# Optimization experiments

Measured on AMD Instinct MI355X. Metric: run time of the kernel, lower is better.

Reference implementation:

```python
import jax, jax.numpy as jnp
import numpy as np
from jax import lax

B, A, H, W = 64, 8, 64, 128
T_EXP = 32
ACTION_HORIZON = 64
DS = 1.0          # reward_cfg['ds']
TEMPERATURE = 0.1 # policy_kwargs['temperature'], method='sharpen'
FOV_HALF_ANGLE_DEG = 35.0
FOV_MAX_RANGE = 100


def _build_buffers():
    # per-action 3x3 one-hot transition kernels: weight 1.0 at 'center' cell,
    # 0.0 at left/right cells (as in MaxEntIRL.__init__ with policy_method='pp')
    center = [[2, 2], [2, 1], [2, 0], [1, 2], [1, 0], [0, 2], [0, 1], [0, 0]]
    tp = np.zeros((A, 1, 3, 3), np.float32)
    for i, (r, c) in enumerate(center):
        tp[i, 0, r, c] = 1.0
    # trapezoidal FOV mask built on a (2H, W) grid, then cropped to first H rows
    rows = np.arange(2 * H, dtype=np.float32)[:, None]
    cols = np.arange(W, dtype=np.float32)[None, :]
    half = np.tan(np.deg2rad(FOV_HALF_ANGLE_DEG)) * rows
    mask = ((np.abs(cols - (W - 1) / 2.0) <= half) & (rows <= FOV_MAX_RANGE))
    fov = mask.astype(np.float32)[:H][None, None]  # (1,1,H,W)
    dyn = np.array([[-1, -1], [-1, 0], [-1, 1], [0, -1],
                    [0, 1], [1, -1], [1, 0], [1, 1]], np.int32)
    return jnp.asarray(tp), jnp.asarray(fov), jnp.asarray(dyn)


def setup_inputs() -> dict:
    key = jax.random.key(0)
    k1, k2 = jax.random.split(key)
    policy = jax.random.normal(k1, (B, A, H, W), jnp.float32)
    # expert SE(2)-like poses; only [:, :, :2, 2] translations are read.
    # Scale to [0,100) so grid cells spread over the map before clamping.
    expert = jax.random.uniform(k2, (B, T_EXP, 3, 3), jnp.float32) * 100.0
    tp, fov, dyn = _build_buffers()
    return {"policy": policy, "expert": expert, "transition_probs": tp,
            "fov_mask": fov, "dynamics": dyn, "action_horizon": ACTION_HORIZON}


def reference(policy, expert, transition_probs, fov_mask, dynamics, action_horizon):
    Bn, An, Hn, Wn = policy.shape
    n_states = Hn * Wn
    barange = jnp.arange(Bn)

    # expert poses -> clamped grid cells  (S: (B, T, 2))
    S = jnp.floor_divide(expert[:, :, :2, 2], DS).astype(jnp.int32)
    S = jnp.stack([jnp.clip(S[..., 0], 0, Hn - 1),
                   jnp.clip(S[..., 1], 0, Wn - 1)], axis=-1)

    # earliest pose inside FOV (argmax of bool gives first True, else 0)
    mask2d = fov_mask[0, 0]
    in_fov = mask2d[S[..., 0], S[..., 1]] > 0  # (B, T)
    idx0 = jnp.argmax(in_fov, axis=1)
    S0c = S[barange, idx0]     # (B, 2) start cell
    S1c = S[:, -1]             # (B, 2) terminal cell
    S0 = S0c[:, 0] * Wn + S0c[:, 1]
    S1 = S1c[:, 0] * Wn + S1c[:, 1]

    # sharpen policy over action dim (stable softmax with temperature)
    logits = (policy - jnp.max(policy, axis=1, keepdims=True)) / TEMPERATURE
    policy_2d = jax.nn.softmax(logits, axis=1)  # (B, A, H, W)

    mu0 = jnp.zeros((Bn, n_states), jnp.float32).at[barange, S0].set(1.0)

    def step(carry, _):
        prev, total = carry
        # zero_terminal_state: kill visitation mass at the terminal cell
        prev_z = prev.at[barange, S1].set(0.0)
        pm = policy_2d * prev_z.reshape(Bn, 1, Hn, Wn)  # (B, A, H, W)
        new = lax.conv_general_dilated(
            pm, transition_probs, window_strides=(1, 1),
            padding=[(1, 1), (1, 1)],
            dimension_numbers=("NCHW", "OIHW", "NCHW"),
            feature_group_count=An)
        new = jnp.sum(new, axis=1).reshape(Bn, n_states)
        return (new, total + prev_z), None

    (last, total), _ = lax.scan(step, (mu0, jnp.zeros_like(mu0)),
                                None, length=action_horizon - 1)
    mu = (total + last).reshape(Bn, Hn, Wn)

    # greedy rollout (torch runs this under no_grad)
    policy_flat = policy.reshape(Bn, An, n_states)
    most_likely_action = jnp.argmax(policy_flat, axis=1)  # (B, n_states)
    most_likely_action = lax.stop_gradient(most_likely_action)

    def roll(St, _):
        a = most_likely_action[barange, St]
        coord = jnp.stack([St // Wn, St % Wn], axis=1) + dynamics[a]
        coord = jnp.stack([jnp.clip(coord[:, 0], 0, Hn - 1),
                           jnp.clip(coord[:, 1], 0, Wn - 1)], axis=1)
        return coord[:, 0] * Wn + coord[:, 1], coord

    _, coords = lax.scan(roll, S0, None, length=action_horizon - 1)  # (T-1,B,2)
    states = jnp.concatenate([S0c[None].astype(coords.dtype), coords],
                             axis=0).transpose(1, 0, 2)  # (B, T, 2)
    bidx = jnp.broadcast_to(barange[:, None], (Bn, action_horizon))
    states_grid = jnp.zeros((Bn, Hn, Wn), jnp.float32).at[
        bidx, states[..., 0], states[..., 1]].add(1.0)
    return mu, states_grid, states
```

## Files before the change

kernel.cpp:

```cpp
#include <hip/hip_runtime.h>

#define THREADS 512

typedef unsigned int u32;

constexpr int BN = 64, AN = 8, HN = 64, WN = 128;
constexpr int HWN = HN * WN;
constexpr int TEXP = 32, AH = 64;
constexpr int PSTR = 136, PROWS = 66;
constexpr int PGUARD = 8;
constexpr int PBUF = PGUARD + PROWS * PSTR;
constexpr size_t LDS_BYTES = (size_t)AN * HWN * 2;

constexpr int GYc[8] = { 1, 1, 1, 0, 0, -1, -1, -1 };
constexpr int GXc[8] = { 1, 0, -1, 1, -1, 1, 0, -1 };

typedef _Float16 h2 __attribute__((ext_vector_type(2)));

union V4 { uint4 q; u32 u[4]; h2 p[4]; _Float16 h[8]; };

__device__ __forceinline__ u32 ab16(u32 hi, u32 lo) {
    return (u32)((((unsigned long long)hi << 32) | lo) >> 16);
}

__device__ __forceinline__ void shiftLR(const V4& d, u32 eLhi, u32 eRlo, V4& L, V4& R) {
    u32 m1 = ab16(d.u[1], d.u[0]);
    u32 m2 = ab16(d.u[2], d.u[1]);
    u32 m3 = ab16(d.u[3], d.u[2]);
    L.u[0] = ab16(d.u[0], eLhi); L.u[1] = m1; L.u[2] = m2; L.u[3] = m3;
    R.u[0] = m1; R.u[1] = m2; R.u[2] = m3; R.u[3] = ab16(eRlo, d.u[3]);
}

extern "C" __global__ __launch_bounds__(THREADS, 2)
void maxent_fused(const float* __restrict__ policy,
                  const float* __restrict__ expert,
                  const float* __restrict__ fovm,
                  const int*   __restrict__ dyn,
                  float* __restrict__ out)
{
    (void)dyn;
    extern __shared__ char smem[];
    const int tid  = threadIdx.x;
    const int lane = tid & 63;
    const bool isScan = blockIdx.x < BN;
    const int b = isScan ? (int)blockIdx.x : (int)blockIdx.x - BN;

    int Sr = 0, Sc = 0; bool infov = false;
    if (lane < TEXP) {
        float e0 = expert[b * (TEXP * 9) + lane * 9 + 2];
        float e1 = expert[b * (TEXP * 9) + lane * 9 + 5];
        int r = (int)floorf(e0); r = r < 0 ? 0 : (r > HN - 1 ? HN - 1 : r);
        int c = (int)floorf(e1); c = c < 0 ? 0 : (c > WN - 1 ? WN - 1 : c);
        Sr = r; Sc = c;
        infov = fovm[r * WN + c] > 0.0f;
    }
    unsigned long long fmask = __ballot(infov);
    int idx0 = fmask ? (__ffsll(fmask) - 1) : 0;
    const int S0r = __shfl(Sr, idx0), S0c = __shfl(Sc, idx0);
    const int S1r = __shfl(Sr, TEXP - 1), S1c = __shfl(Sc, TEXP - 1);
    const bool S0eqS1 = (S0r == S1r) && (S0c == S1c);

    if (isScan) {
        _Float16* Pl = (_Float16*)smem;

        const float* pb = policy + (size_t)b * AN * HWN;
        #pragma unroll
        for (int kk = 0; kk < 4; ++kk) {
            const int pix = (kk * THREADS + tid) * 4;
            float v[8][4];
            float m[4] = {-3.4e38f, -3.4e38f, -3.4e38f, -3.4e38f};
            #pragma unroll
            for (int a = 0; a < 8; ++a) {
                float4 f = *(const float4*)(pb + a * HWN + pix);
                v[a][0] = f.x; v[a][1] = f.y; v[a][2] = f.z; v[a][3] = f.w;
                m[0] = fmaxf(m[0], f.x); m[1] = fmaxf(m[1], f.y);
                m[2] = fmaxf(m[2], f.z); m[3] = fmaxf(m[3], f.w);
            }
            float s[4] = {0.f, 0.f, 0.f, 0.f};
            #pragma unroll
            for (int a = 0; a < 8; ++a)
                #pragma unroll
                for (int j = 0; j < 4; ++j) { v[a][j] = __expf((v[a][j] - m[j]) * 10.0f); s[j] += v[a][j]; }
            float inv[4];
            #pragma unroll
            for (int j = 0; j < 4; ++j) inv[j] = 1.0f / s[j];
            #pragma unroll
            for (int a = 0; a < 8; ++a) {
                u32 lo = (u32)__builtin_bit_cast(unsigned short, (_Float16)(v[a][0] * inv[0]))
                       | ((u32)__builtin_bit_cast(unsigned short, (_Float16)(v[a][1] * inv[1])) << 16);
                u32 hi = (u32)__builtin_bit_cast(unsigned short, (_Float16)(v[a][2] * inv[2]))
                       | ((u32)__builtin_bit_cast(unsigned short, (_Float16)(v[a][3] * inv[3])) << 16);
                uint2 pk2; pk2.x = lo; pk2.y = hi;
                *(uint2*)(Pl + a * HWN + pix) = pk2;
            }
        }
        __syncthreads();

        const int wv = tid >> 6;
        const int y0 = 8 * wv + 2 * (lane >> 4);
        const int x0 = (lane & 15) * 8;
        const bool edgeL = (lane & 15) == 0;
        const bool edgeR = (lane & 15) == 15;

        V4 pa0[8], pa1[8];
        #pragma unroll
        for (int a = 0; a < 8; ++a) {
            const int gy = GYc[a], gx = GXc[a];
            #pragma unroll
            for (int r = 0; r < 2; ++r) {
                const int ny = y0 + r + gy;
                V4 wvv;
                #pragma unroll
                for (int k = 0; k < 8; ++k) wvv.h[k] = (_Float16)0.0f;
                if (ny >= 0 && ny < HN) {
                    const _Float16* base = Pl + a * HWN + ny * WN + x0;
                    V4 qq; qq.q = *(const uint4*)base;
                    if (gx == 0) {
                        wvv = qq;
                    } else if (gx == 1) {
                        _Float16 e = (x0 < WN - 8) ? base[8] : base[7];
                        #pragma unroll
                        for (int k = 0; k < 7; ++k) wvv.h[k] = qq.h[k + 1];
                        wvv.h[7] = e;
                    } else {
                        _Float16 e = (x0 > 0) ? base[-1] : base[0];
                        wvv.h[0] = e;
                        #pragma unroll
                        for (int k = 1; k < 8; ++k) wvv.h[k] = qq.h[k - 1];
                    }
                }
                if (r == 0) pa0[a] = wvv; else pa1[a] = wvv;
            }
        }
        __syncthreads();

        _Float16* B0 = (_Float16*)smem;
        _Float16* B1 = B0 + PBUF;
        for (int i = tid; i < 2 * PBUF; i += THREADS) B0[i] = (_Float16)0.0f;
        __syncthreads();
        if (tid == 0 && !S0eqS1) B0[PGUARD + (S0r + 1) * PSTR + S0c] = (_Float16)1.0f;
        __syncthreads();

        const bool own0 = (y0     == S1r) && (S1c >= x0) && (S1c < x0 + 8);
        const bool own1 = (y0 + 1 == S1r) && (S1c >= x0) && (S1c < x0 + 8);
        V4 zA, zB, sA, sB;
        #pragma unroll
        for (int q = 0; q < 4; ++q) {
            u32 mA = ~0u, mB = ~0u;
            if (own0 && ((S1c - x0) >> 1) == q) mA = ((S1c - x0) & 1) ? 0x0000FFFFu : 0xFFFF0000u;
            if (own1 && ((S1c - x0) >> 1) == q) mB = ((S1c - x0) & 1) ? 0x0000FFFFu : 0xFFFF0000u;
            zA.u[q] = mA; zB.u[q] = mB;
            u32 v0 = 0;
            if (!S0eqS1 && y0 == S0r && S0c >= x0 && S0c < x0 + 8 && ((S0c - x0) >> 1) == q)
                v0 = ((S0c - x0) & 1) ? 0x3C000000u : 0x00003C00u;
            u32 v1 = 0;
            if (!S0eqS1 && y0 + 1 == S0r && S0c >= x0 && S0c < x0 + 8 && ((S0c - x0) >> 1) == q)
                v1 = ((S0c - x0) & 1) ? 0x3C000000u : 0x00003C00u;
            sA.u[q] = v0; sB.u[q] = v1;
        }

        float total[16];
        #pragma unroll
        for (int k = 0; k < 16; ++k) total[k] = 0.f;
        V4 nnA, nnB;
        #pragma unroll
        for (int q = 0; q < 4; ++q) { nnA.u[q] = 0; nnB.u[q] = 0; }

        const int offT  = PGUARD + y0 * PSTR + x0;
        const int offD  = offT + 3 * PSTR;
        const int offW0 = offT + PSTR;
        const int offW1 = offW0 + PSTR;

        _Float16* RB = B0; _Float16* WB = B1;
        for (int it = 0; it < AH - 1; ++it) {
            const bool active = (8 * wv <= S0r + it + 1) && (8 * wv + 7 >= S0r - it - 1);
            if (active) {
                V4 qT, qD;
                qT.q = *(const uint4*)(RB + offT);
                qD.q = *(const uint4*)(RB + offD);

                #pragma unroll
                for (int q = 0; q < 4; ++q) {
                    total[2*q]     += (float)sA.p[q].x;
                    total[2*q + 1] += (float)sA.p[q].y;
                    total[8 + 2*q]     += (float)sB.p[q].x;
                    total[8 + 2*q + 1] += (float)sB.p[q].y;
                }

                u32 packL_AB = (sA.u[3] >> 16) | (sB.u[3] & 0xFFFF0000u);
                u32 packR_AB = (sA.u[0] & 0xFFFFu) | (sB.u[0] << 16);
                u32 packL_TD = (qT.u[3] >> 16) | (qD.u[3] & 0xFFFF0000u);
                u32 packR_TD = (qT.u[0] & 0xFFFFu) | (qD.u[0] << 16);
                u32 pLab = (u32)__shfl((int)packL_AB, (lane - 1) & 63); pLab = edgeL ? 0u : pLab;
                u32 pRab = (u32)__shfl((int)packR_AB, (lane + 1) & 63); pRab = edgeR ? 0u : pRab;
                u32 pLtd = (u32)__shfl((int)packL_TD, (lane - 1) & 63); pLtd = edgeL ? 0u : pLtd;
                u32 pRtd = (u32)__shfl((int)packR_TD, (lane + 1) & 63); pRtd = edgeR ? 0u : pRtd;

                V4 TL, TR, AL, AR, BL, BR, DL, DR;
                shiftLR(qT, pLtd << 16,          pRtd & 0xFFFFu, TL, TR);
                shiftLR(qD, pLtd & 0xFFFF0000u,  pRtd >> 16,     DL, DR);
                shiftLR(sA, pLab << 16,          pRab & 0xFFFFu, AL, AR);
                shiftLR(sB, pLab & 0xFFFF0000u,  pRab >> 16,     BL, BR);

                #pragma unroll
                for (int q = 0; q < 4; ++q) { nnA.u[q] = 0; nnB.u[q] = 0; }
                #define ACC(dst, pa, src) \
                    _Pragma("unroll") for (int q = 0; q < 4; ++q) dst.p[q] += pa.p[q] * src.p[q];
                ACC(nnA, pa0[0], BR) ACC(nnA, pa0[1], sB) ACC(nnA, pa0[2], BL)
                ACC(nnA, pa0[3], AR)                       ACC(nnA, pa0[4], AL)
                ACC(nnA, pa0[5], TR) ACC(nnA, pa0[6], qT) ACC(nnA, pa0[7], TL)
                ACC(nnB, pa1[0], DR) ACC(nnB, pa1[1], qD) ACC(nnB, pa1[2], DL)
                ACC(nnB, pa1[3], BR)                       ACC(nnB, pa1[4], BL)
                ACC(nnB, pa1[5], AR) ACC(nnB, pa1[6], sA) ACC(nnB, pa1[7], AL)
                #undef ACC

                #pragma unroll
                for (int q = 0; q < 4; ++q) {
                    sA.u[q] = nnA.u[q] & zA.u[q];
                    sB.u[q] = nnB.u[q] & zB.u[q];
                }
                *(uint4*)(WB + offW0) = sA.q;
                *(uint4*)(WB + offW1) = sB.q;
            }
            __syncthreads();
            _Float16* t = RB; RB = WB; WB = t;
        }

        float* ob0 = out + (size_t)b * HWN + y0 * WN + x0;
        float* ob1 = ob0 + WN;
        #pragma unroll
        for (int k = 0; k < 8; ++k) {
            ob0[k] = total[k]     + (float)nnA.h[k];
            ob1[k] = total[8 + k] + (float)nnB.h[k];
        }

    } else {
        short* amap = (short*)smem;
        float* grid = (float*)(smem + 16384);
        const float* pb = policy + (size_t)b * AN * HWN;
        #pragma unroll
        for (int c = 0; c < 4; ++c) {
            const int pix = (c * THREADS + tid) * 4;
            float4 f0 = *(const float4*)(pb + pix);
            float b0 = f0.x, b1 = f0.y, b2 = f0.z, b3 = f0.w;
            int a0 = 0, a1 = 0, a2 = 0, a3 = 0;
            #pragma unroll
            for (int a = 1; a < 8; ++a) {
                float4 f = *(const float4*)(pb + a * HWN + pix);
                if (f.x > b0) { b0 = f.x; a0 = a; }
                if (f.y > b1) { b1 = f.y; a1 = a; }
                if (f.z > b2) { b2 = f.z; a2 = a; }
                if (f.w > b3) { b3 = f.w; a3 = a; }
            }
            uint2 pk2;
            pk2.x = (u32)a0 | ((u32)a1 << 16);
            pk2.y = (u32)a2 | ((u32)a3 << 16);
            *(uint2*)(amap + pix) = pk2;
        }
        for (int i = tid; i < HWN; i += THREADS) grid[i] = 0.f;
        __syncthreads();

        if (tid == 0) {
            float* so = out + 2 * (size_t)HWN * BN + b * (AH * 2);
            int cr = S0r, cc = S0c;
            so[0] = (float)cr; so[1] = (float)cc;
            grid[cr * WN + cc] += 1.0f;
            for (int t = 1; t < AH; ++t) {
                const int a = amap[cr * WN + cc];
                const int dr = (a < 3) ? -1 : ((a < 5) ? 0 : 1);
                int dc;
                if (a < 3) dc = a - 1;
                else if (a == 3) dc = -1;
                else if (a == 4) dc = 1;
                else dc = a - 6;
                cr += dr; cc += dc;
                cr = cr < 0 ? 0 : (cr > HN - 1 ? HN - 1 : cr);
                cc = cc < 0 ? 0 : (cc > WN - 1 ? WN - 1 : cc);
                so[t * 2] = (float)cr; so[t * 2 + 1] = (float)cc;
                grid[cr * WN + cc] += 1.0f;
            }
        }
        __syncthreads();
        float* sg = out + (size_t)HWN * BN + b * HWN;
        for (int i = tid; i < HWN; i += THREADS) sg[i] = grid[i];
    }
}

extern "C" void kernel_launch(void* const* d_in, const int* in_sizes, int n_in,
                              void* d_out, int out_size, void* d_ws, size_t ws_size,
                              hipStream_t stream) {
    const float* policy = (const float*)d_in[0];
    const float* expert = (const float*)d_in[1];
    const float* fovm   = (const float*)d_in[3];
    const int*   dyn    = (const int*)d_in[4];
    float* out = (float*)d_out;

    (void)hipFuncSetAttribute((const void*)maxent_fused,
                              hipFuncAttributeMaxDynamicSharedMemorySize,
                              (int)LDS_BYTES);
    hipLaunchKernelGGL(maxent_fused, dim3(2 * BN), dim3(THREADS), LDS_BYTES, stream,
                       policy, expert, fovm, dyn, out);
}
```

Baseline: 56.40 us.

## Use DPP row shifts and precompute own-band stencil terms before the barrier

The cross-lane neighbour exchanges in the recurrence loop switch from __shfl to DPP row_shr/row_shl with bound_ctrl zeroing, which also handles the 16-lane row edges. The stencil contributions that depend only on the thread's own two rows are computed right after the store, before the barrier, so only the terms that need the neighbour rows (loaded from LDS) stay on the path after the barrier. Per-step totals are now summed in fp16 and flushed to fp32 every four steps, which removes conversions but adds fp16 rounding error to the accumulated totals.

```diff
diff --git a/kernel.cpp b/kernel.cpp
--- a/kernel.cpp
+++ b/kernel.cpp
@@ -29,6 +29,13 @@
     u32 m3 = ab16(d.u[3], d.u[2]);
     L.u[0] = ab16(d.u[0], eLhi); L.u[1] = m1; L.u[2] = m2; L.u[3] = m3;
     R.u[0] = m1; R.u[1] = m2; R.u[2] = m3; R.u[3] = ab16(eRlo, d.u[3]);
+}
+
+__device__ __forceinline__ u32 dpp_from_left(u32 x) {
+    return (u32)__builtin_amdgcn_update_dpp(0, (int)x, 0x111 , 0xf, 0xf, true);
+}
+__device__ __forceinline__ u32 dpp_from_right(u32 x) {
+    return (u32)__builtin_amdgcn_update_dpp(0, (int)x, 0x101 , 0xf, 0xf, true);
 }
 
 extern "C" __global__ __launch_bounds__(THREADS, 2)
@@ -99,8 +106,6 @@
         const int wv = tid >> 6;
         const int y0 = 8 * wv + 2 * (lane >> 4);
         const int x0 = (lane & 15) * 8;
-        const bool edgeL = (lane & 15) == 0;
-        const bool edgeR = (lane & 15) == 15;
 
         V4 pa0[8], pa1[8];
         #pragma unroll
@@ -162,14 +167,38 @@
         float total[16];
         #pragma unroll
         for (int k = 0; k < 16; ++k) total[k] = 0.f;
-        V4 nnA, nnB;
-        #pragma unroll
-        for (int q = 0; q < 4; ++q) { nnA.u[q] = 0; nnB.u[q] = 0; }
+        V4 nnA, nnB, tA, tB;
+        #pragma unroll
+        for (int q = 0; q < 4; ++q) { nnA.u[q] = 0; nnB.u[q] = 0; tA.u[q] = 0; tB.u[q] = 0; }
 
         const int offT  = PGUARD + y0 * PSTR + x0;
         const int offD  = offT + 3 * PSTR;
         const int offW0 = offT + PSTR;
         const int offW1 = offW0 + PSTR;
+
+        #define COMPUTE_OWN(ownA_, ownB_)                                              \
+        {                                                                              \
+            u32 packL = (sA.u[3] >> 16) | (sB.u[3] & 0xFFFF0000u);                     \
+            u32 packR = (sA.u[0] & 0xFFFFu) | (sB.u[0] << 16);                         \
+            u32 pL = dpp_from_left(packL);                                             \
+            u32 pR = dpp_from_right(packR);                                            \
+            V4 AL, AR, BL, BR;                                                         \
+            shiftLR(sA, pL << 16,          pR & 0xFFFFu, AL, AR);                      \
+            shiftLR(sB, pL & 0xFFFF0000u,  pR >> 16,     BL, BR);                      \
+            _Pragma("unroll")                                                          \
+            for (int q = 0; q < 4; ++q) {                                              \
+                h2 a = pa0[0].p[q] * BR.p[q]; a += pa0[1].p[q] * sB.p[q];              \
+                a += pa0[2].p[q] * BL.p[q];   a += pa0[3].p[q] * AR.p[q];              \
+                a += pa0[4].p[q] * AL.p[q];                                            \
+                h2 bb = pa1[3].p[q] * BR.p[q]; bb += pa1[4].p[q] * BL.p[q];            \
+                bb += pa1[5].p[q] * AR.p[q];   bb += pa1[6].p[q] * sA.p[q];            \
+                bb += pa1[7].p[q] * AL.p[q];                                           \
+                ownA_.p[q] = a; ownB_.p[q] = bb;                                       \
+            }                                                                          \
+        }
+
+        V4 ownA, ownB;
+        COMPUTE_OWN(ownA, ownB)
 
         _Float16* RB = B0; _Float16* WB = B1;
         for (int it = 0; it < AH - 1; ++it) {
@@ -180,51 +209,42 @@
                 qD.q = *(const uint4*)(RB + offD);
 
                 #pragma unroll
-                for (int q = 0; q < 4; ++q) {
-                    total[2*q]     += (float)sA.p[q].x;
-                    total[2*q + 1] += (float)sA.p[q].y;
-                    total[8 + 2*q]     += (float)sB.p[q].x;
-                    total[8 + 2*q + 1] += (float)sB.p[q].y;
+                for (int q = 0; q < 4; ++q) { tA.p[q] += sA.p[q]; tB.p[q] += sB.p[q]; }
+                if ((it & 3) == 3 || it == AH - 2) {
+                    #pragma unroll
+                    for (int q = 0; q < 4; ++q) {
+                        total[2*q]       += (float)tA.p[q].x;  total[2*q + 1]     += (float)tA.p[q].y;
+                        total[8 + 2*q]   += (float)tB.p[q].x;  total[8 + 2*q + 1] += (float)tB.p[q].y;
+                        tA.u[q] = 0; tB.u[q] = 0;
+                    }
                 }
 
-                u32 packL_AB = (sA.u[3] >> 16) | (sB.u[3] & 0xFFFF0000u);
-                u32 packR_AB = (sA.u[0] & 0xFFFFu) | (sB.u[0] << 16);
                 u32 packL_TD = (qT.u[3] >> 16) | (qD.u[3] & 0xFFFF0000u);
                 u32 packR_TD = (qT.u[0] & 0xFFFFu) | (qD.u[0] << 16);
-                u32 pLab = (u32)__shfl((int)packL_AB, (lane - 1) & 63); pLab = edgeL ? 0u : pLab;
-                u32 pRab = (u32)__shfl((int)packR_AB, (lane + 1) & 63); pRab = edgeR ? 0u : pRab;
-                u32 pLtd = (u32)__shfl((int)packL_TD, (lane - 1) & 63); pLtd = edgeL ? 0u : pLtd;
-                u32 pRtd = (u32)__shfl((int)packR_TD, (lane + 1) & 63); pRtd = edgeR ? 0u : pRtd;
-
-                V4 TL, TR, AL, AR, BL, BR, DL, DR;
+                u32 pLtd = dpp_from_left(packL_TD);
+                u32 pRtd = dpp_from_right(packR_TD);
+                V4 TL, TR, DL, DR;
                 shiftLR(qT, pLtd << 16,          pRtd & 0xFFFFu, TL, TR);
                 shiftLR(qD, pLtd & 0xFFFF0000u,  pRtd >> 16,     DL, DR);
-                shiftLR(sA, pLab << 16,          pRab & 0xFFFFu, AL, AR);
-                shiftLR(sB, pLab & 0xFFFF0000u,  pRab >> 16,     BL, BR);
-
-                #pragma unroll
-                for (int q = 0; q < 4; ++q) { nnA.u[q] = 0; nnB.u[q] = 0; }
-                #define ACC(dst, pa, src) \
-                    _Pragma("unroll") for (int q = 0; q < 4; ++q) dst.p[q] += pa.p[q] * src.p[q];
-                ACC(nnA, pa0[0], BR) ACC(nnA, pa0[1], sB) ACC(nnA, pa0[2], BL)
-                ACC(nnA, pa0[3], AR)                       ACC(nnA, pa0[4], AL)
-                ACC(nnA, pa0[5], TR) ACC(nnA, pa0[6], qT) ACC(nnA, pa0[7], TL)
-                ACC(nnB, pa1[0], DR) ACC(nnB, pa1[1], qD) ACC(nnB, pa1[2], DL)
-                ACC(nnB, pa1[3], BR)                       ACC(nnB, pa1[4], BL)
-                ACC(nnB, pa1[5], AR) ACC(nnB, pa1[6], sA) ACC(nnB, pa1[7], AL)
-                #undef ACC
-
                 #pragma unroll
                 for (int q = 0; q < 4; ++q) {
+                    h2 a = ownA.p[q] + pa0[5].p[q] * TR.p[q];
+                    a += pa0[6].p[q] * qT.p[q];  a += pa0[7].p[q] * TL.p[q];
+                    h2 bb = ownB.p[q] + pa1[0].p[q] * DR.p[q];
+                    bb += pa1[1].p[q] * qD.p[q]; bb += pa1[2].p[q] * DL.p[q];
+                    nnA.p[q] = a; nnB.p[q] = bb;
                     sA.u[q] = nnA.u[q] & zA.u[q];
                     sB.u[q] = nnB.u[q] & zB.u[q];
                 }
                 *(uint4*)(WB + offW0) = sA.q;
                 *(uint4*)(WB + offW1) = sB.q;
+
+                COMPUTE_OWN(ownA, ownB)
             }
             __syncthreads();
             _Float16* t = RB; RB = WB; WB = t;
         }
+        #undef COMPUTE_OWN
 
         float* ob0 = out + (size_t)b * HWN + y0 * WN + x0;
         float* ob1 = ob0 + WN;
```

New measurement: 52.81 us. 6.4% less time.

## Remap diffusion scan to column-pair lanes with DPP shifts and row-halo LDS exchange

Applied to the files above, without the earlier changes.

Each lane now owns two adjacent columns across eight rows instead of eight columns across two rows. Horizontal neighbours come from DPP wave shifts instead of ds shuffles, and vertical neighbours come from registers within the wave. Only the top and bottom rows of each wave go through a small double-buffered LDS halo instead of a full padded state buffer. Running totals are also accumulated in fp16 for four steps before being flushed to fp32, which saves conversions but loses some precision.

```diff
diff --git a/kernel.cpp b/kernel.cpp
--- a/kernel.cpp
+++ b/kernel.cpp
@@ -3,33 +3,33 @@
 #define THREADS 512
 
 typedef unsigned int u32;
+typedef unsigned long long u64;
 
 constexpr int BN = 64, AN = 8, HN = 64, WN = 128;
 constexpr int HWN = HN * WN;
 constexpr int TEXP = 32, AH = 64;
-constexpr int PSTR = 136, PROWS = 66;
-constexpr int PGUARD = 8;
-constexpr int PBUF = PGUARD + PROWS * PSTR;
 constexpr size_t LDS_BYTES = (size_t)AN * HWN * 2;
 
 constexpr int GYc[8] = { 1, 1, 1, 0, 0, -1, -1, -1 };
 constexpr int GXc[8] = { 1, 0, -1, 1, -1, 1, 0, -1 };
 
 typedef _Float16 h2 __attribute__((ext_vector_type(2)));
-
-union V4 { uint4 q; u32 u[4]; h2 p[4]; _Float16 h[8]; };
+union U { u32 u; h2 p; _Float16 h[2]; };
+
+__device__ __forceinline__ h2  H(u32 x) { U t; t.u = x; return t.p; }
+__device__ __forceinline__ u32 Bc(h2 x) { U t; t.p = x; return t.u; }
 
 __device__ __forceinline__ u32 ab16(u32 hi, u32 lo) {
-    return (u32)((((unsigned long long)hi << 32) | lo) >> 16);
-}
-
-__device__ __forceinline__ void shiftLR(const V4& d, u32 eLhi, u32 eRlo, V4& L, V4& R) {
-    u32 m1 = ab16(d.u[1], d.u[0]);
-    u32 m2 = ab16(d.u[2], d.u[1]);
-    u32 m3 = ab16(d.u[3], d.u[2]);
-    L.u[0] = ab16(d.u[0], eLhi); L.u[1] = m1; L.u[2] = m2; L.u[3] = m3;
-    R.u[0] = m1; R.u[1] = m2; R.u[2] = m3; R.u[3] = ab16(eRlo, d.u[3]);
-}
+    return (u32)((((u64)hi << 32) | lo) >> 16);
+}
+__device__ __forceinline__ u32 wsr1(u32 x) {
+    return (u32)__builtin_amdgcn_update_dpp(0, (int)x, 0x138, 0xf, 0xf, true);
+}
+__device__ __forceinline__ u32 wsl1(u32 x) {
+    return (u32)__builtin_amdgcn_update_dpp(0, (int)x, 0x130, 0xf, 0xf, true);
+}
+__device__ __forceinline__ u32 shL(u32 d) { return ab16(d, wsr1(d)); }
+__device__ __forceinline__ u32 shR(u32 d) { return ab16(wsl1(d), d); }
 
 extern "C" __global__ __launch_bounds__(THREADS, 2)
 void maxent_fused(const float* __restrict__ policy,
@@ -96,142 +96,114 @@
         }
         __syncthreads();
 
-        const int wv = tid >> 6;
-        const int y0 = 8 * wv + 2 * (lane >> 4);
-        const int x0 = (lane & 15) * 8;
-        const bool edgeL = (lane & 15) == 0;
-        const bool edgeR = (lane & 15) == 15;
-
-        V4 pa0[8], pa1[8];
+        const int w = tid >> 6;
+        const int rbase = 8 * w;
+
+        u32 pa[8][8];
         #pragma unroll
         for (int a = 0; a < 8; ++a) {
             const int gy = GYc[a], gx = GXc[a];
             #pragma unroll
-            for (int r = 0; r < 2; ++r) {
-                const int ny = y0 + r + gy;
-                V4 wvv;
-                #pragma unroll
-                for (int k = 0; k < 8; ++k) wvv.h[k] = (_Float16)0.0f;
-                if (ny >= 0 && ny < HN) {
-                    const _Float16* base = Pl + a * HWN + ny * WN + x0;
-                    V4 qq; qq.q = *(const uint4*)base;
-                    if (gx == 0) {
-                        wvv = qq;
-                    } else if (gx == 1) {
-                        _Float16 e = (x0 < WN - 8) ? base[8] : base[7];
-                        #pragma unroll
-                        for (int k = 0; k < 7; ++k) wvv.h[k] = qq.h[k + 1];
-                        wvv.h[7] = e;
-                    } else {
-                        _Float16 e = (x0 > 0) ? base[-1] : base[0];
-                        wvv.h[0] = e;
-                        #pragma unroll
-                        for (int k = 1; k < 8; ++k) wvv.h[k] = qq.h[k - 1];
+            for (int r = 0; r < 8; ++r) {
+                const int sr = rbase + r + gy;
+                u32 d = 0;
+                if (sr >= 0 && sr < HN)
+                    d = *(const u32*)(Pl + a * HWN + sr * WN + 2 * lane);
+                pa[a][r] = (gx == 0) ? d : ((gx == 1) ? shR(d) : shL(d));
+            }
+        }
+        __syncthreads();
+
+        u32* hx = (u32*)smem;
+        for (int i = tid; i < 2048; i += THREADS) hx[i] = 0;
+
+        u32 s[8], zm[8];
+        #pragma unroll
+        for (int r = 0; r < 8; ++r) {
+            const int gr = rbase + r;
+            s[r] = (!S0eqS1 && gr == S0r && (S0c >> 1) == lane)
+                     ? ((S0c & 1) ? 0x3C000000u : 0x00003C00u) : 0u;
+            zm[r] = ~0u;
+            if (gr == S1r && (S1c >> 1) == lane)
+                zm[r] = (S1c & 1) ? 0x0000FFFFu : 0xFFFF0000u;
+        }
+        __syncthreads();
+        hx[(2 * w + 0) * 64 + lane] = s[0];
+        hx[(2 * w + 1) * 64 + lane] = s[7];
+        __syncthreads();
+
+        u32 t16[8], nn[8];
+        float tot[16];
+        #pragma unroll
+        for (int r = 0; r < 8; ++r) { t16[r] = 0; nn[r] = 0; }
+        #pragma unroll
+        for (int k = 0; k < 16; ++k) tot[k] = 0.f;
+
+        const int rdT = (2 * w - 1) * 64 + lane;
+        const int rdD = (2 * w + 2) * 64 + lane;
+        const int wr0 = (2 * w + 0) * 64 + lane;
+        const int wr7 = (2 * w + 1) * 64 + lane;
+
+        for (int it = 0; it < AH - 1; ++it) {
+            const int pb_ = (it & 1) << 10;
+            const int wb_ = 1024 - pb_;
+            const bool active = (rbase <= S0r + it + 1) && (rbase + 7 >= S0r - it - 1);
+            if (active) {
+                const u32 hT = (w > 0) ? hx[pb_ + rdT] : 0u;
+                const u32 hD = (w < 7) ? hx[pb_ + rdD] : 0u;
+
+                #pragma unroll
+                for (int r = 0; r < 8; ++r) t16[r] = Bc(H(t16[r]) + H(s[r]));
+                if ((it & 3) == 3 || it == AH - 2) {
+                    #pragma unroll
+                    for (int r = 0; r < 8; ++r) {
+                        tot[2*r]   += (float)H(t16[r]).x;
+                        tot[2*r+1] += (float)H(t16[r]).y;
+                        t16[r] = 0;
                     }
                 }
-                if (r == 0) pa0[a] = wvv; else pa1[a] = wvv;
-            }
-        }
-        __syncthreads();
-
-        _Float16* B0 = (_Float16*)smem;
-        _Float16* B1 = B0 + PBUF;
-        for (int i = tid; i < 2 * PBUF; i += THREADS) B0[i] = (_Float16)0.0f;
-        __syncthreads();
-        if (tid == 0 && !S0eqS1) B0[PGUARD + (S0r + 1) * PSTR + S0c] = (_Float16)1.0f;
-        __syncthreads();
-
-        const bool own0 = (y0     == S1r) && (S1c >= x0) && (S1c < x0 + 8);
-        const bool own1 = (y0 + 1 == S1r) && (S1c >= x0) && (S1c < x0 + 8);
-        V4 zA, zB, sA, sB;
-        #pragma unroll
-        for (int q = 0; q < 4; ++q) {
-            u32 mA = ~0u, mB = ~0u;
-            if (own0 && ((S1c - x0) >> 1) == q) mA = ((S1c - x0) & 1) ? 0x0000FFFFu : 0xFFFF0000u;
-            if (own1 && ((S1c - x0) >> 1) == q) mB = ((S1c - x0) & 1) ? 0x0000FFFFu : 0xFFFF0000u;
-            zA.u[q] = mA; zB.u[q] = mB;
-            u32 v0 = 0;
-            if (!S0eqS1 && y0 == S0r && S0c >= x0 && S0c < x0 + 8 && ((S0c - x0) >> 1) == q)
-                v0 = ((S0c - x0) & 1) ? 0x3C000000u : 0x00003C00u;
-            u32 v1 = 0;
-            if (!S0eqS1 && y0 + 1 == S0r && S0c >= x0 && S0c < x0 + 8 && ((S0c - x0) >> 1) == q)
-                v1 = ((S0c - x0) & 1) ? 0x3C000000u : 0x00003C00u;
-            sA.u[q] = v0; sB.u[q] = v1;
-        }
-
-        float total[16];
-        #pragma unroll
-        for (int k = 0; k < 16; ++k) total[k] = 0.f;
-        V4 nnA, nnB;
-        #pragma unroll
-        for (int q = 0; q < 4; ++q) { nnA.u[q] = 0; nnB.u[q] = 0; }
-
-        const int offT  = PGUARD + y0 * PSTR + x0;
-        const int offD  = offT + 3 * PSTR;
-        const int offW0 = offT + PSTR;
-        const int offW1 = offW0 + PSTR;
-
-        _Float16* RB = B0; _Float16* WB = B1;
-        for (int it = 0; it < AH - 1; ++it) {
-            const bool active = (8 * wv <= S0r + it + 1) && (8 * wv + 7 >= S0r - it - 1);
-            if (active) {
-                V4 qT, qD;
-                qT.q = *(const uint4*)(RB + offT);
-                qD.q = *(const uint4*)(RB + offD);
-
-                #pragma unroll
-                for (int q = 0; q < 4; ++q) {
-                    total[2*q]     += (float)sA.p[q].x;
-                    total[2*q + 1] += (float)sA.p[q].y;
-                    total[8 + 2*q]     += (float)sB.p[q].x;
-                    total[8 + 2*q + 1] += (float)sB.p[q].y;
+
+                u32 L[8], R[8];
+                #pragma unroll
+                for (int r = 0; r < 8; ++r) { L[r] = shL(s[r]); R[r] = shR(s[r]); }
+
+                u32 ns[8];
+                constexpr int RO[8] = {1, 2, 3, 4, 5, 6, 0, 7};
+                #pragma unroll
+                for (int ri = 0; ri < 8; ++ri) {
+                    const int r = RO[ri];
+                    const u32 cm1 = (r == 0) ? hT      : s[r - 1];
+                    const u32 lm1 = (r == 0) ? shL(hT) : L[r - 1];
+                    const u32 rm1 = (r == 0) ? shR(hT) : R[r - 1];
+                    const u32 cp1 = (r == 7) ? hD      : s[r + 1];
+                    const u32 lp1 = (r == 7) ? shL(hD) : L[r + 1];
+                    const u32 rp1 = (r == 7) ? shR(hD) : R[r + 1];
+                    h2 acc =  H(pa[0][r]) * H(rp1);
+                    acc += H(pa[1][r]) * H(cp1);
+                    acc += H(pa[2][r]) * H(lp1);
+                    acc += H(pa[3][r]) * H(R[r]);
+                    acc += H(pa[4][r]) * H(L[r]);
+                    acc += H(pa[5][r]) * H(rm1);
+                    acc += H(pa[6][r]) * H(cm1);
+                    acc += H(pa[7][r]) * H(lm1);
+                    nn[r] = Bc(acc);
+                    ns[r] = nn[r] & zm[r];
                 }
-
-                u32 packL_AB = (sA.u[3] >> 16) | (sB.u[3] & 0xFFFF0000u);
-                u32 packR_AB = (sA.u[0] & 0xFFFFu) | (sB.u[0] << 16);
-                u32 packL_TD = (qT.u[3] >> 16) | (qD.u[3] & 0xFFFF0000u);
-                u32 packR_TD = (qT.u[0] & 0xFFFFu) | (qD.u[0] << 16);
-                u32 pLab = (u32)__shfl((int)packL_AB, (lane - 1) & 63); pLab = edgeL ? 0u : pLab;
-                u32 pRab = (u32)__shfl((int)packR_AB, (lane + 1) & 63); pRab = edgeR ? 0u : pRab;
-                u32 pLtd = (u32)__shfl((int)packL_TD, (lane - 1) & 63); pLtd = edgeL ? 0u : pLtd;
-                u32 pRtd = (u32)__shfl((int)packR_TD, (lane + 1) & 63); pRtd = edgeR ? 0u : pRtd;
-
-                V4 TL, TR, AL, AR, BL, BR, DL, DR;
-                shiftLR(qT, pLtd << 16,          pRtd & 0xFFFFu, TL, TR);
-                shiftLR(qD, pLtd & 0xFFFF0000u,  pRtd >> 16,     DL, DR);
-                shiftLR(sA, pLab << 16,          pRab & 0xFFFFu, AL, AR);
-                shiftLR(sB, pLab & 0xFFFF0000u,  pRab >> 16,     BL, BR);
-
-                #pragma unroll
-                for (int q = 0; q < 4; ++q) { nnA.u[q] = 0; nnB.u[q] = 0; }
-                #define ACC(dst, pa, src) \
-                    _Pragma("unroll") for (int q = 0; q < 4; ++q) dst.p[q] += pa.p[q] * src.p[q];
-                ACC(nnA, pa0[0], BR) ACC(nnA, pa0[1], sB) ACC(nnA, pa0[2], BL)
-                ACC(nnA, pa0[3], AR)                       ACC(nnA, pa0[4], AL)
-                ACC(nnA, pa0[5], TR) ACC(nnA, pa0[6], qT) ACC(nnA, pa0[7], TL)
-                ACC(nnB, pa1[0], DR) ACC(nnB, pa1[1], qD) ACC(nnB, pa1[2], DL)
-                ACC(nnB, pa1[3], BR)                       ACC(nnB, pa1[4], BL)
-                ACC(nnB, pa1[5], AR) ACC(nnB, pa1[6], sA) ACC(nnB, pa1[7], AL)
-                #undef ACC
-
-                #pragma unroll
-                for (int q = 0; q < 4; ++q) {
-                    sA.u[q] = nnA.u[q] & zA.u[q];
-                    sB.u[q] = nnB.u[q] & zB.u[q];
-                }
-                *(uint4*)(WB + offW0) = sA.q;
-                *(uint4*)(WB + offW1) = sB.q;
+                #pragma unroll
+                for (int r = 0; r < 8; ++r) s[r] = ns[r];
+
+                hx[wb_ + wr0] = s[0];
+                hx[wb_ + wr7] = s[7];
             }
             __syncthreads();
-            _Float16* t = RB; RB = WB; WB = t;
-        }
-
-        float* ob0 = out + (size_t)b * HWN + y0 * WN + x0;
-        float* ob1 = ob0 + WN;
-        #pragma unroll
-        for (int k = 0; k < 8; ++k) {
-            ob0[k] = total[k]     + (float)nnA.h[k];
-            ob1[k] = total[8 + k] + (float)nnB.h[k];
+        }
+
+        #pragma unroll
+        for (int r = 0; r < 8; ++r) {
+            float2 f;
+            f.x = tot[2*r]   + (float)H(nn[r]).x;
+            f.y = tot[2*r+1] + (float)H(nn[r]).y;
+            *(float2*)(out + (size_t)b * HWN + (rbase + r) * WN + 2 * lane) = f;
         }
 
     } else {
```

Measured after the change: 49.01 us. -13.1%, faster.
